# Kernel tuning notes

Hardware: AMD Instinct MI355X
Metric: run time of the kernel (lower is better)

The kernel has to match this reference:

```python
import jax, jax.numpy as jnp
import numpy as np

N, E, HID, HEADS, EDIM = 32768, 262144, 64, 4, 3
C = HID  # per-head out channels (concat=False -> mean over heads)


def setup_inputs() -> dict:
    key = jax.random.key(0)
    ks = jax.random.split(key, 24)
    g = lambda k, shape, s=1.0: jax.random.normal(k, shape, jnp.float32) * s
    s_lin = 1.0 / np.sqrt(HID)
    s_edge = 1.0 / np.sqrt(EDIM)
    s_att = 1.0 / np.sqrt(C)
    inp = {
        "t": jnp.zeros((1,), jnp.float32),
        "h": g(ks[0], (N, HID)),
        "edge_index": jax.random.randint(ks[1], (2, E), 0, N, jnp.int32),
        "edge_attr": g(ks[2], (E, EDIM)),
        "W1": g(ks[3], (HID, HEADS * C), s_lin),
        "We1": g(ks[4], (EDIM, HEADS * C), s_edge),
        "att_src1": g(ks[5], (HEADS, C), s_att),
        "att_dst1": g(ks[6], (HEADS, C), s_att),
        "att_edge1": g(ks[7], (HEADS, C), s_att),
        "b1": jnp.zeros((C,), jnp.float32),
        "ln_g1": jnp.ones((HID,), jnp.float32),
        "ln_b1": jnp.zeros((HID,), jnp.float32),
        # last GAT layer's lin weight is scaled by 0.1 in __init__
        "W2": g(ks[8], (HID, HEADS * C), s_lin) * 0.1,
        "We2": g(ks[9], (EDIM, HEADS * C), s_edge),
        "att_src2": g(ks[10], (HEADS, C), s_att),
        "att_dst2": g(ks[11], (HEADS, C), s_att),
        "att_edge2": g(ks[12], (HEADS, C), s_att),
        "b2": jnp.zeros((C,), jnp.float32),
        "ln_g2": jnp.ones((HID,), jnp.float32),
        "ln_b2": jnp.zeros((HID,), jnp.float32),
    }
    return inp


def _gat_layer(z, src, dst, edge_attr, W, We, a_src, a_dst, a_edge, b):
    # PyG GATConv(edge_dim>0, concat=False, add_self_loops=False), eval mode (no dropout)
    x = (z @ W).reshape(-1, HEADS, C)                      # [N,H,C]
    alpha_s = jnp.einsum("nhc,hc->nh", x, a_src)           # [N,H]
    alpha_d = jnp.einsum("nhc,hc->nh", x, a_dst)           # [N,H]
    e = (edge_attr @ We).reshape(-1, HEADS, C)             # [E,H,C]
    alpha_e = jnp.einsum("ehc,hc->eh", e, a_edge)          # [E,H]
    logit = jax.nn.leaky_relu(alpha_s[src] + alpha_d[dst] + alpha_e, 0.2)  # [E,H]
    # segment softmax over incoming edges of each destination node
    m = jax.lax.stop_gradient(jax.ops.segment_max(logit, dst, num_segments=N))
    ex = jnp.exp(logit - m[dst])
    denom = jax.ops.segment_sum(ex, dst, num_segments=N)
    alpha = ex / (denom[dst] + 1e-16)                      # [E,H]
    msg = x[src] * alpha[..., None]                        # [E,H,C] gather + weight
    out = jax.ops.segment_sum(msg, dst, num_segments=N)    # [N,H,C] scatter-add
    return out.mean(axis=1) + b                            # head mean + bias -> [N,C]


def _layernorm(x, g, b, eps=1e-5):
    mu = x.mean(-1, keepdims=True)
    var = ((x - mu) ** 2).mean(-1, keepdims=True)
    return (x - mu) * jax.lax.rsqrt(var + eps) * g + b


def reference(t, h, edge_index, edge_attr, W1, We1, att_src1, att_dst1, att_edge1, b1,
              ln_g1, ln_b1, W2, We2, att_src2, att_dst2, att_edge2, b2, ln_g2, ln_b2):
    del t  # autonomous ODE func: t unused
    src, dst = edge_index[0], edge_index[1]
    z = h
    z = jax.nn.silu(_layernorm(_gat_layer(z, src, dst, edge_attr, W1, We1, att_src1, att_dst1, att_edge1, b1), ln_g1, ln_b1))
    z = jax.nn.silu(_layernorm(_gat_layer(z, src, dst, edge_attr, W2, We2, att_src2, att_dst2, att_edge2, b2), ln_g2, ln_b2))
    return z
```

## Files before the change

### kernel.cpp

```cpp
#include <hip/hip_runtime.h>
#include <math.h>

#define HIDDEN 64
#define HEADS 4
#define HC 256
#define CAP 64

typedef __attribute__((ext_vector_type(8))) short short8;
typedef __attribute__((ext_vector_type(4))) float f32x4;

__device__ __forceinline__ unsigned short f2bf(float f) {
    unsigned int u = __float_as_uint(f);
    u += 0x7fffu + ((u >> 16) & 1u);
    return (unsigned short)(u >> 16);
}

__device__ __forceinline__ unsigned short f2h(float f) {
    _Float16 h = (_Float16)f;
    return *(unsigned short*)&h;
}

__device__ __forceinline__ float h2f(unsigned int u) {
    unsigned short s = (unsigned short)u;
    _Float16 h = *(_Float16*)&s;
    return (float)h;
}

__device__ __forceinline__ float bflo(unsigned int u) { return __uint_as_float(u << 16); }
__device__ __forceinline__ float bfhi(unsigned int u) { return __uint_as_float(u & 0xffff0000u); }

__global__ __launch_bounds__(256) void k_fused(const int* __restrict__ dst,
                                               const int* __restrict__ src,
                                               const float* __restrict__ ea,
                                               const float* __restrict__ h,
                                               const float* __restrict__ W1f,
                                               const float* __restrict__ W2f,
                                               const float* __restrict__ We1,
                                               const float* __restrict__ ae1,
                                               const float* __restrict__ We2,
                                               const float* __restrict__ ae2,
                                               const float* __restrict__ ats1,
                                               const float* __restrict__ atd1,
                                               const float* __restrict__ ats2,
                                               const float* __restrict__ atd2,
                                               int* __restrict__ counts,
                                               uint2* __restrict__ eb,
                                               ushort* __restrict__ zb,
                                               ushort* __restrict__ wst1,
                                               ushort* __restrict__ wst2,
                                               float* __restrict__ wsv,
                                               float* __restrict__ wr, int E) {
    int t = threadIdx.x, b = blockIdx.x;
    if (b < 1024) {
        int e = b * 256 + t;
        if (e < E) {
            int d = dst[e];
            int c = atomicAdd(&counts[d], 1);
            if (c < CAP) {
                size_t slot = (size_t)d * CAP + c;
                unsigned int lo = (unsigned int)(src[e] & 0xffff)
                                | ((unsigned int)f2h(ea[e * 3 + 0]) << 16);
                unsigned int hi = (unsigned int)f2h(ea[e * 3 + 1])
                                | ((unsigned int)f2h(ea[e * 3 + 2]) << 16);
                eb[slot] = make_uint2(lo, hi);
            }
        }
    } else if (b < 3072) {
        int i = (b - 1024) * 256 + t;
        float4 v = ((const float4*)h)[i];
        ushort4 o;
        o.x = f2bf(v.x); o.y = f2bf(v.y); o.z = f2bf(v.z); o.w = f2bf(v.w);
        ((ushort4*)zb)[i] = o;
    } else if (b < 3200) {
        int j = (b - 3072) * 256 + t;
        const float* W = (j < 16384) ? W1f : W2f;
        ushort* wst = (j < 16384) ? wst1 : wst2;
        int i = j & 16383;
        int c = i >> 8, k = i & 255;
        wst[i] = f2bf(0.25f * W[(k & 63) * HC + (k >> 6) * 64 + c]);
    } else if (b < 3204) {
        int r = b - 3200;
        const float* W = (r >> 1) ? W2f : W1f;
        const float* at;
        if (r == 0) at = ats1; else if (r == 1) at = atd1;
        else if (r == 2) at = ats2; else at = atd2;
        int hh = t >> 6, k = t & 63;
        const float4* wrow = (const float4*)&W[k * HC + hh * 64];
        const float4* arow = (const float4*)&at[hh * 64];
        float v = 0.f;
#pragma unroll
        for (int c4 = 0; c4 < 16; ++c4) {
            float4 wv = wrow[c4], av = arow[c4];
            v += wv.x * av.x + wv.y * av.y + wv.z * av.z + wv.w * av.w;
        }
        wsv[r * 256 + hh * 64 + k] = v;
    } else {
        int wv = t >> 6, lane = t & 63;
#pragma unroll
        for (int it = 0; it < 6; ++it) {
            int comb = wv + it * 4;
            int layer = comb / 12;
            int dh = comb % 12;
            int d = dh >> 2, hh = dh & 3;
            const float* We = layer ? We2 : We1;
            const float* at = layer ? ae2 : ae1;
            float v = We[d * HC + hh * HIDDEN + lane] * at[hh * HIDDEN + lane];
            for (int o = 32; o > 0; o >>= 1) v += __shfl_down(v, o);
            if (lane == 0) wr[layer * 16 + d * HEADS + hh] = v;
        }
    }
}

__global__ __launch_bounds__(256) void k_alpha(const ushort* __restrict__ zb,
                                               const float* __restrict__ wsv,
                                               float* __restrict__ as_,
                                               float* __restrict__ ad_) {
    __shared__ float ls[512];
    int t = threadIdx.x;
    ls[t] = wsv[t];
    ls[t + 256] = wsv[t + 256];
    __syncthreads();
    int n = blockIdx.x * 256 + t;
    const ushort* zr = zb + (size_t)n * HIDDEN;
    float as[4] = {0.f, 0.f, 0.f, 0.f};
    float ad[4] = {0.f, 0.f, 0.f, 0.f};
#pragma unroll
    for (int ks = 0; ks < 8; ++ks) {
        uint4 v = *(const uint4*)(zr + ks * 8);
        unsigned int uu[4] = {v.x, v.y, v.z, v.w};
#pragma unroll
        for (int p = 0; p < 4; ++p) {
            float f0 = bflo(uu[p]), f1 = bfhi(uu[p]);
            int k = ks * 8 + p * 2;
#pragma unroll
            for (int hh = 0; hh < 4; ++hh) {
                as[hh] += f0 * ls[hh * 64 + k] + f1 * ls[hh * 64 + k + 1];
                ad[hh] += f0 * ls[256 + hh * 64 + k] + f1 * ls[256 + hh * 64 + k + 1];
            }
        }
    }
    *(float4*)&as_[n * 4] = make_float4(as[0], as[1], as[2], as[3]);
    *(float4*)&ad_[n * 4] = make_float4(ad[0], ad[1], ad[2], ad[3]);
}

__global__ __launch_bounds__(256) void k_aggregate(
        const ushort* __restrict__ zb, const uint2* __restrict__ eb,
        const int* __restrict__ counts,
        const float* __restrict__ as_, const float* __restrict__ ad_,
        const float* __restrict__ wrl,
        ushort* __restrict__ agg, int N) {
    int lane = threadIdx.x & 63;
    int h = lane >> 4, sub = lane & 15;
    int wid = blockIdx.x * 4 + (threadIdx.x >> 6);
    int nwaves = gridDim.x * 4;
    float w0 = wrl[h], w1 = wrl[4 + h], w2 = wrl[8 + h];

    for (int n = wid; n < N; n += nwaves) {
        int deg = counts[n];
        if (deg > CAP) deg = CAP;
        size_t base = (size_t)n * CAP;
        float ad4 = ad_[n * 4 + h];
        float ssum = 0.f;
        float acc0 = 0.f, acc1 = 0.f, acc2 = 0.f, acc3 = 0.f;

        for (int cs = 0; cs < deg; cs += 16) {
            int idx = cs + sub;
            int s_sub = 0;
            float wgt = 0.f;
            if (idx < deg) {
                uint2 rec = eb[base + idx];
                s_sub = (int)(rec.x & 0xffffu);
                float lg = as_[s_sub * 4 + h] + ad4
                         + h2f(rec.x >> 16) * w0
                         + h2f(rec.y) * w1
                         + h2f(rec.y >> 16) * w2;
                lg = (lg >= 0.f) ? lg : 0.2f * lg;
                wgt = __expf(lg);
            }
            ssum += wgt;

            int jb = deg - cs; if (jb > 16) jb = 16;
            for (int j = 0; j < jb; j += 4) {
                int s_g = __shfl(s_sub, j + h);
                uint2 zv = *(const uint2*)&zb[(size_t)s_g * HIDDEN + sub * 4];
#pragma unroll
                for (int e = 0; e < 4; ++e) {
                    float we = __shfl(wgt, h * 16 + j + e);
                    unsigned int zx = (unsigned int)__shfl((int)zv.x, e * 16 + sub);
                    unsigned int zy = (unsigned int)__shfl((int)zv.y, e * 16 + sub);
                    acc0 += we * bflo(zx);
                    acc1 += we * bfhi(zx);
                    acc2 += we * bflo(zy);
                    acc3 += we * bfhi(zy);
                }
            }
        }
#pragma unroll
        for (int o = 1; o < 16; o <<= 1) ssum += __shfl_xor(ssum, o);
        float winv = 1.f / (ssum + 1e-16f);
        uint2 o2;
        o2.x = (unsigned)f2bf(acc0 * winv) | ((unsigned)f2bf(acc1 * winv) << 16);
        o2.y = (unsigned)f2bf(acc2 * winv) | ((unsigned)f2bf(acc3 * winv) << 16);
        *(uint2*)&agg[(size_t)n * HC + h * 64 + sub * 4] = o2;
    }
}

__global__ __launch_bounds__(256) void k_out(const ushort* __restrict__ agg,
                                             const ushort* __restrict__ wst,
                                             const float* __restrict__ bias,
                                             const float* __restrict__ lng,
                                             const float* __restrict__ lnb,
                                             const float* __restrict__ wsv2,
                                             float* __restrict__ as_,
                                             float* __restrict__ ad_,
                                             float* __restrict__ outf,
                                             ushort* __restrict__ outb) {
    int lane = threadIdx.x & 63;
    int q = lane & 15, quad = lane >> 4;
    int row0 = blockIdx.x * 64 + (threadIdx.x >> 6) * 16;

    const ushort* arow = agg + (size_t)(row0 + q) * HC + quad * 8;
    short8 a[8];
#pragma unroll
    for (int ks = 0; ks < 8; ++ks) a[ks] = *(const short8*)(arow + ks * 32);

    f32x4 acc[4];
#pragma unroll
    for (int nt = 0; nt < 4; ++nt) {
        const ushort* brow = wst + (size_t)(nt * 16 + q) * HC + quad * 8;
        f32x4 c4 = {0.f, 0.f, 0.f, 0.f};
#pragma unroll
        for (int ks = 0; ks < 8; ++ks) {
            short8 bfr = *(const short8*)(brow + ks * 32);
            c4 = __builtin_amdgcn_mfma_f32_16x16x32_bf16(a[ks], bfr, c4, 0, 0, 0);
        }
        acc[nt] = c4;
    }

    float u[4][4], s1[4] = {0.f, 0.f, 0.f, 0.f};
#pragma unroll
    for (int nt = 0; nt < 4; ++nt) {
        float bv = bias[nt * 16 + q];
#pragma unroll
        for (int r = 0; r < 4; ++r) { u[nt][r] = acc[nt][r] + bv; s1[r] += u[nt][r]; }
    }
#pragma unroll
    for (int o = 1; o < 16; o <<= 1)
#pragma unroll
        for (int r = 0; r < 4; ++r) s1[r] += __shfl_xor(s1[r], o);
    float mu[4], s2[4] = {0.f, 0.f, 0.f, 0.f};
#pragma unroll
    for (int r = 0; r < 4; ++r) mu[r] = s1[r] * (1.f / 64.f);
#pragma unroll
    for (int nt = 0; nt < 4; ++nt)
#pragma unroll
        for (int r = 0; r < 4; ++r) { float d = u[nt][r] - mu[r]; s2[r] += d * d; }
#pragma unroll
    for (int o = 1; o < 16; o <<= 1)
#pragma unroll
        for (int r = 0; r < 4; ++r) s2[r] += __shfl_xor(s2[r], o);
    float rstd[4];
#pragma unroll
    for (int r = 0; r < 4; ++r) rstd[r] = rsqrtf(s2[r] * (1.f / 64.f) + 1e-5f);

    float rv[4][4];
#pragma unroll
    for (int nt = 0; nt < 4; ++nt) {
        float gv = lng[nt * 16 + q], bb = lnb[nt * 16 + q];
#pragma unroll
        for (int r = 0; r < 4; ++r) {
            float y = (u[nt][r] - mu[r]) * rstd[r] * gv + bb;
            rv[nt][r] = y / (1.f + __expf(-y));
        }
    }

    if (outb) {
#pragma unroll
        for (int nt = 0; nt < 4; ++nt)
#pragma unroll
            for (int r = 0; r < 4; ++r)
                outb[(size_t)(row0 + quad * 4 + r) * HIDDEN + nt * 16 + q] = f2bf(rv[nt][r]);
        float vs[4][4] = {{0.f}}, vd[4][4] = {{0.f}};
#pragma unroll
        for (int hh = 0; hh < 4; ++hh)
#pragma unroll
            for (int nt = 0; nt < 4; ++nt) {
                float wsc = wsv2[hh * 64 + nt * 16 + q];
                float wdc = wsv2[256 + hh * 64 + nt * 16 + q];
#pragma unroll
                for (int r = 0; r < 4; ++r) {
                    vs[r][hh] += rv[nt][r] * wsc;
                    vd[r][hh] += rv[nt][r] * wdc;
                }
            }
#pragma unroll
        for (int o = 1; o < 16; o <<= 1)
#pragma unroll
            for (int r = 0; r < 4; ++r)
#pragma unroll
                for (int hh = 0; hh < 4; ++hh) {
                    vs[r][hh] += __shfl_xor(vs[r][hh], o);
                    vd[r][hh] += __shfl_xor(vd[r][hh], o);
                }
        if (q < 4) {
#pragma unroll
            for (int r = 0; r < 4; ++r) {
                float sv = (q == 0) ? vs[r][0] : (q == 1) ? vs[r][1]
                         : (q == 2) ? vs[r][2] : vs[r][3];
                float dv = (q == 0) ? vd[r][0] : (q == 1) ? vd[r][1]
                         : (q == 2) ? vd[r][2] : vd[r][3];
                int n = row0 + quad * 4 + r;
                as_[n * 4 + q] = sv;
                ad_[n * 4 + q] = dv;
            }
        }
    } else {
#pragma unroll
        for (int nt = 0; nt < 4; ++nt)
#pragma unroll
            for (int r = 0; r < 4; ++r)
                outf[(size_t)(row0 + quad * 4 + r) * HIDDEN + nt * 16 + q] = rv[nt][r];
    }
}


extern "C" void kernel_launch(void* const* d_in, const int* in_sizes, int n_in,
                              void* d_out, int out_size, void* d_ws, size_t ws_size,
                              hipStream_t stream) {
    const float* h   = (const float*)d_in[1];
    const int*   ei  = (const int*)d_in[2];
    const float* ea  = (const float*)d_in[3];
    const float* W1  = (const float*)d_in[4];
    const float* We1 = (const float*)d_in[5];
    const float* as1 = (const float*)d_in[6];
    const float* ad1 = (const float*)d_in[7];
    const float* ae1 = (const float*)d_in[8];
    const float* b1  = (const float*)d_in[9];
    const float* lg1 = (const float*)d_in[10];
    const float* lb1 = (const float*)d_in[11];
    const float* W2  = (const float*)d_in[12];
    const float* We2 = (const float*)d_in[13];
    const float* as2 = (const float*)d_in[14];
    const float* ad2 = (const float*)d_in[15];
    const float* ae2 = (const float*)d_in[16];
    const float* b2  = (const float*)d_in[17];
    const float* lg2 = (const float*)d_in[18];
    const float* lb2 = (const float*)d_in[19];

    const int N = in_sizes[1] / HIDDEN;
    const int E = in_sizes[2] / 2;
    const int* srcp = ei;
    const int* dstp = ei + E;

    char* w = (char*)d_ws;
    ushort* agg   = (ushort*)w; w += (size_t)N * HC * 2;
    ushort* zb    = (ushort*)w; w += (size_t)N * HIDDEN * 2;
    float* as_    = (float*)w;  w += (size_t)N * HEADS * 4;
    float* adv    = (float*)w;  w += (size_t)N * HEADS * 4;
    ushort* wst1  = (ushort*)w; w += 16384 * 2;
    ushort* wst2  = (ushort*)w; w += 16384 * 2;
    float* wsv    = (float*)w;  w += 1024 * 4;
    float* wr     = (float*)w;  w += 128;
    int* counts   = (int*)w;    w += (size_t)N * 4;
    uint2* eb     = (uint2*)w;  w += (size_t)N * CAP * 8;

    hipMemsetAsync(counts, 0, (size_t)N * 4, stream);
    k_fused<<<3205, 256, 0, stream>>>(dstp, srcp, ea, h, W1, W2,
                                      We1, ae1, We2, ae2,
                                      as1, ad1, as2, ad2,
                                      counts, eb, zb, wst1, wst2, wsv, wr, E);

    k_alpha<<<N / 256, 256, 0, stream>>>(zb, wsv, as_, adv);
    k_aggregate<<<4096, 256, 0, stream>>>(zb, eb, counts, as_, adv, wr, agg, N);
    k_out<<<N / 64, 256, 0, stream>>>(agg, wst1, b1, lg1, lb1, wsv + 512,
                                      as_, adv, nullptr, zb);
    k_aggregate<<<4096, 256, 0, stream>>>(zb, eb, counts, as_, adv, wr + 16, agg, N);
    k_out<<<N / 64, 256, 0, stream>>>(agg, wst2, b2, lg2, lb2, nullptr,
                                      nullptr, nullptr, (float*)d_out, nullptr);
}
```

Baseline: 194.0 us.

## Fuse edge aggregation with output projection and LayerNorm via shared-memory tile

Merges the aggregate and output kernels into one kernel per layer. Each block aggregates 16 nodes into an LDS tile, then one wave runs the MFMA projection, LayerNorm, SiLU and next-layer alpha computation. This drops the large global agg buffer write and read, and ping-pongs the z and alpha buffers so the fused kernel can run without read/write hazards. The aggregation inner loop also changes: each lane now gathers one neighbor row per step and accumulates all four heads, followed by cross-head shuffle reductions. Only one of four waves does the epilogue, so MFMA work is serialized per block and occupancy may be limited by the launch bound.

```diff
diff --git a/kernel.cpp b/kernel.cpp
--- a/kernel.cpp
+++ b/kernel.cpp
@@ -143,25 +143,46 @@
     *(float4*)&ad_[n * 4] = make_float4(ad[0], ad[1], ad[2], ad[3]);
 }
 
-__global__ __launch_bounds__(256) void k_aggregate(
+__global__ __launch_bounds__(256, 4) void k_aggout(
         const ushort* __restrict__ zb, const uint2* __restrict__ eb,
         const int* __restrict__ counts,
         const float* __restrict__ as_, const float* __restrict__ ad_,
         const float* __restrict__ wrl,
-        ushort* __restrict__ agg, int N) {
+        const ushort* __restrict__ wst, const float* __restrict__ bias,
+        const float* __restrict__ lng, const float* __restrict__ lnb,
+        const float* __restrict__ wsv2,
+        float* __restrict__ as2, float* __restrict__ ad2,
+        float* __restrict__ outf, ushort* __restrict__ outb, int N) {
+    __shared__ ushort sagg[16][264];
     int lane = threadIdx.x & 63;
+    int wave = threadIdx.x >> 6;
     int h = lane >> 4, sub = lane & 15;
-    int wid = blockIdx.x * 4 + (threadIdx.x >> 6);
-    int nwaves = gridDim.x * 4;
+    int nbase = blockIdx.x * 16;
+
     float w0 = wrl[h], w1 = wrl[4 + h], w2 = wrl[8 + h];
 
-    for (int n = wid; n < N; n += nwaves) {
-        int deg = counts[n];
-        if (deg > CAP) deg = CAP;
+    int degs[4]; float ad4s[4];
+#pragma unroll
+    for (int i = 0; i < 4; ++i) {
+        int n = nbase + wave * 4 + i;
+        int d = counts[n];
+        degs[i] = (d > CAP) ? CAP : d;
+        ad4s[i] = ad_[(size_t)n * 4 + h];
+    }
+
+#pragma unroll
+    for (int i = 0; i < 4; ++i) {
+        int nl = wave * 4 + i;
+        int n = nbase + nl;
+        int deg = degs[i];
         size_t base = (size_t)n * CAP;
-        float ad4 = ad_[n * 4 + h];
+        float ad4 = ad4s[i];
         float ssum = 0.f;
-        float acc0 = 0.f, acc1 = 0.f, acc2 = 0.f, acc3 = 0.f;
+        float acc[4][4];
+#pragma unroll
+        for (int a = 0; a < 4; ++a)
+#pragma unroll
+            for (int j = 0; j < 4; ++j) acc[a][j] = 0.f;
 
         for (int cs = 0; cs < deg; cs += 16) {
             int idx = cs + sub;
@@ -170,7 +191,7 @@
             if (idx < deg) {
                 uint2 rec = eb[base + idx];
                 s_sub = (int)(rec.x & 0xffffu);
-                float lg = as_[s_sub * 4 + h] + ad4
+                float lg = as_[(size_t)s_sub * 4 + h] + ad4
                          + h2f(rec.x >> 16) * w0
                          + h2f(rec.y) * w1
                          + h2f(rec.y >> 16) * w2;
@@ -180,146 +201,148 @@
             ssum += wgt;
 
             int jb = deg - cs; if (jb > 16) jb = 16;
-            for (int j = 0; j < jb; j += 4) {
-                int s_g = __shfl(s_sub, j + h);
+            for (int j4 = 0; j4 < jb; j4 += 4) {
+                int eidx = j4 + h;
+                int s_g = __shfl(s_sub, eidx);
                 uint2 zv = *(const uint2*)&zb[(size_t)s_g * HIDDEN + sub * 4];
-#pragma unroll
-                for (int e = 0; e < 4; ++e) {
-                    float we = __shfl(wgt, h * 16 + j + e);
-                    unsigned int zx = (unsigned int)__shfl((int)zv.x, e * 16 + sub);
-                    unsigned int zy = (unsigned int)__shfl((int)zv.y, e * 16 + sub);
-                    acc0 += we * bflo(zx);
-                    acc1 += we * bfhi(zx);
-                    acc2 += we * bflo(zy);
-                    acc3 += we * bfhi(zy);
+                float z0 = bflo(zv.x), z1 = bfhi(zv.x);
+                float z2v = bflo(zv.y), z3 = bfhi(zv.y);
+#pragma unroll
+                for (int hh = 0; hh < 4; ++hh) {
+                    float wh = __shfl(wgt, hh * 16 + eidx);
+                    acc[hh][0] += wh * z0;
+                    acc[hh][1] += wh * z1;
+                    acc[hh][2] += wh * z2v;
+                    acc[hh][3] += wh * z3;
                 }
             }
         }
 #pragma unroll
         for (int o = 1; o < 16; o <<= 1) ssum += __shfl_xor(ssum, o);
         float winv = 1.f / (ssum + 1e-16f);
-        uint2 o2;
-        o2.x = (unsigned)f2bf(acc0 * winv) | ((unsigned)f2bf(acc1 * winv) << 16);
-        o2.y = (unsigned)f2bf(acc2 * winv) | ((unsigned)f2bf(acc3 * winv) << 16);
-        *(uint2*)&agg[(size_t)n * HC + h * 64 + sub * 4] = o2;
+#pragma unroll
+        for (int a = 0; a < 4; ++a)
+#pragma unroll
+            for (int j = 0; j < 4; ++j) {
+                acc[a][j] += __shfl_xor(acc[a][j], 16);
+                acc[a][j] += __shfl_xor(acc[a][j], 32);
+            }
+        float sel[4];
+#pragma unroll
+        for (int j = 0; j < 4; ++j)
+            sel[j] = (h == 0) ? acc[0][j] : (h == 1) ? acc[1][j]
+                   : (h == 2) ? acc[2][j] : acc[3][j];
+        uint2 pk;
+        pk.x = (unsigned)f2bf(sel[0] * winv) | ((unsigned)f2bf(sel[1] * winv) << 16);
+        pk.y = (unsigned)f2bf(sel[2] * winv) | ((unsigned)f2bf(sel[3] * winv) << 16);
+        *(uint2*)&sagg[nl][h * 64 + sub * 4] = pk;
     }
-}
-
-__global__ __launch_bounds__(256) void k_out(const ushort* __restrict__ agg,
-                                             const ushort* __restrict__ wst,
-                                             const float* __restrict__ bias,
-                                             const float* __restrict__ lng,
-                                             const float* __restrict__ lnb,
-                                             const float* __restrict__ wsv2,
-                                             float* __restrict__ as_,
-                                             float* __restrict__ ad_,
-                                             float* __restrict__ outf,
-                                             ushort* __restrict__ outb) {
-    int lane = threadIdx.x & 63;
-    int q = lane & 15, quad = lane >> 4;
-    int row0 = blockIdx.x * 64 + (threadIdx.x >> 6) * 16;
-
-    const ushort* arow = agg + (size_t)(row0 + q) * HC + quad * 8;
-    short8 a[8];
-#pragma unroll
-    for (int ks = 0; ks < 8; ++ks) a[ks] = *(const short8*)(arow + ks * 32);
-
-    f32x4 acc[4];
-#pragma unroll
-    for (int nt = 0; nt < 4; ++nt) {
-        const ushort* brow = wst + (size_t)(nt * 16 + q) * HC + quad * 8;
-        f32x4 c4 = {0.f, 0.f, 0.f, 0.f};
-#pragma unroll
-        for (int ks = 0; ks < 8; ++ks) {
-            short8 bfr = *(const short8*)(brow + ks * 32);
-            c4 = __builtin_amdgcn_mfma_f32_16x16x32_bf16(a[ks], bfr, c4, 0, 0, 0);
-        }
-        acc[nt] = c4;
-    }
-
-    float u[4][4], s1[4] = {0.f, 0.f, 0.f, 0.f};
-#pragma unroll
-    for (int nt = 0; nt < 4; ++nt) {
-        float bv = bias[nt * 16 + q];
-#pragma unroll
-        for (int r = 0; r < 4; ++r) { u[nt][r] = acc[nt][r] + bv; s1[r] += u[nt][r]; }
-    }
-#pragma unroll
-    for (int o = 1; o < 16; o <<= 1)
-#pragma unroll
-        for (int r = 0; r < 4; ++r) s1[r] += __shfl_xor(s1[r], o);
-    float mu[4], s2[4] = {0.f, 0.f, 0.f, 0.f};
-#pragma unroll
-    for (int r = 0; r < 4; ++r) mu[r] = s1[r] * (1.f / 64.f);
-#pragma unroll
-    for (int nt = 0; nt < 4; ++nt)
-#pragma unroll
-        for (int r = 0; r < 4; ++r) { float d = u[nt][r] - mu[r]; s2[r] += d * d; }
-#pragma unroll
-    for (int o = 1; o < 16; o <<= 1)
-#pragma unroll
-        for (int r = 0; r < 4; ++r) s2[r] += __shfl_xor(s2[r], o);
-    float rstd[4];
-#pragma unroll
-    for (int r = 0; r < 4; ++r) rstd[r] = rsqrtf(s2[r] * (1.f / 64.f) + 1e-5f);
-
-    float rv[4][4];
-#pragma unroll
-    for (int nt = 0; nt < 4; ++nt) {
-        float gv = lng[nt * 16 + q], bb = lnb[nt * 16 + q];
-#pragma unroll
-        for (int r = 0; r < 4; ++r) {
-            float y = (u[nt][r] - mu[r]) * rstd[r] * gv + bb;
-            rv[nt][r] = y / (1.f + __expf(-y));
-        }
-    }
-
-    if (outb) {
+    __syncthreads();
+
+    if (wave == 0) {
+        int q = lane & 15, quad = lane >> 4;
+        short8 a[8];
+#pragma unroll
+        for (int ks = 0; ks < 8; ++ks)
+            a[ks] = *(const short8*)&sagg[q][quad * 8 + ks * 32];
+
+        f32x4 acc[4];
+#pragma unroll
+        for (int nt = 0; nt < 4; ++nt) {
+            const ushort* brow = wst + (size_t)(nt * 16 + q) * HC + quad * 8;
+            f32x4 c4 = {0.f, 0.f, 0.f, 0.f};
+#pragma unroll
+            for (int ks = 0; ks < 8; ++ks) {
+                short8 bfr = *(const short8*)(brow + ks * 32);
+                c4 = __builtin_amdgcn_mfma_f32_16x16x32_bf16(a[ks], bfr, c4, 0, 0, 0);
+            }
+            acc[nt] = c4;
+        }
+
+        float u[4][4], s1[4] = {0.f, 0.f, 0.f, 0.f};
+#pragma unroll
+        for (int nt = 0; nt < 4; ++nt) {
+            float bv = bias[nt * 16 + q];
+#pragma unroll
+            for (int r = 0; r < 4; ++r) { u[nt][r] = acc[nt][r] + bv; s1[r] += u[nt][r]; }
+        }
+#pragma unroll
+        for (int o = 1; o < 16; o <<= 1)
+#pragma unroll
+            for (int r = 0; r < 4; ++r) s1[r] += __shfl_xor(s1[r], o);
+        float mu[4], s2[4] = {0.f, 0.f, 0.f, 0.f};
+#pragma unroll
+        for (int r = 0; r < 4; ++r) mu[r] = s1[r] * (1.f / 64.f);
 #pragma unroll
         for (int nt = 0; nt < 4; ++nt)
 #pragma unroll
-            for (int r = 0; r < 4; ++r)
-                outb[(size_t)(row0 + quad * 4 + r) * HIDDEN + nt * 16 + q] = f2bf(rv[nt][r]);
-        float vs[4][4] = {{0.f}}, vd[4][4] = {{0.f}};
-#pragma unroll
-        for (int hh = 0; hh < 4; ++hh)
-#pragma unroll
-            for (int nt = 0; nt < 4; ++nt) {
-                float wsc = wsv2[hh * 64 + nt * 16 + q];
-                float wdc = wsv2[256 + hh * 64 + nt * 16 + q];
+            for (int r = 0; r < 4; ++r) { float d = u[nt][r] - mu[r]; s2[r] += d * d; }
+#pragma unroll
+        for (int o = 1; o < 16; o <<= 1)
+#pragma unroll
+            for (int r = 0; r < 4; ++r) s2[r] += __shfl_xor(s2[r], o);
+        float rstd[4];
+#pragma unroll
+        for (int r = 0; r < 4; ++r) rstd[r] = rsqrtf(s2[r] * (1.f / 64.f) + 1e-5f);
+
+        float rv[4][4];
+#pragma unroll
+        for (int nt = 0; nt < 4; ++nt) {
+            float gv = lng[nt * 16 + q], bb = lnb[nt * 16 + q];
+#pragma unroll
+            for (int r = 0; r < 4; ++r) {
+                float y = (u[nt][r] - mu[r]) * rstd[r] * gv + bb;
+                rv[nt][r] = y / (1.f + __expf(-y));
+            }
+        }
+
+        if (outb) {
+#pragma unroll
+            for (int nt = 0; nt < 4; ++nt)
+#pragma unroll
+                for (int r = 0; r < 4; ++r)
+                    outb[(size_t)(nbase + quad * 4 + r) * HIDDEN + nt * 16 + q] = f2bf(rv[nt][r]);
+            float vs[4][4] = {{0.f}}, vd[4][4] = {{0.f}};
+#pragma unroll
+            for (int hh = 0; hh < 4; ++hh)
+#pragma unroll
+                for (int nt = 0; nt < 4; ++nt) {
+                    float wsc = wsv2[hh * 64 + nt * 16 + q];
+                    float wdc = wsv2[256 + hh * 64 + nt * 16 + q];
+#pragma unroll
+                    for (int r = 0; r < 4; ++r) {
+                        vs[r][hh] += rv[nt][r] * wsc;
+                        vd[r][hh] += rv[nt][r] * wdc;
+                    }
+                }
+#pragma unroll
+            for (int o = 1; o < 16; o <<= 1)
+#pragma unroll
+                for (int r = 0; r < 4; ++r)
+#pragma unroll
+                    for (int hh = 0; hh < 4; ++hh) {
+                        vs[r][hh] += __shfl_xor(vs[r][hh], o);
+                        vd[r][hh] += __shfl_xor(vd[r][hh], o);
+                    }
+            if (q < 4) {
 #pragma unroll
                 for (int r = 0; r < 4; ++r) {
-                    vs[r][hh] += rv[nt][r] * wsc;
-                    vd[r][hh] += rv[nt][r] * wdc;
+                    float sv = (q == 0) ? vs[r][0] : (q == 1) ? vs[r][1]
+                             : (q == 2) ? vs[r][2] : vs[r][3];
+                    float dv = (q == 0) ? vd[r][0] : (q == 1) ? vd[r][1]
+                             : (q == 2) ? vd[r][2] : vd[r][3];
+                    int n = nbase + quad * 4 + r;
+                    as2[(size_t)n * 4 + q] = sv;
+                    ad2[(size_t)n * 4 + q] = dv;
                 }
             }
-#pragma unroll
-        for (int o = 1; o < 16; o <<= 1)
-#pragma unroll
-            for (int r = 0; r < 4; ++r)
-#pragma unroll
-                for (int hh = 0; hh < 4; ++hh) {
-                    vs[r][hh] += __shfl_xor(vs[r][hh], o);
-                    vd[r][hh] += __shfl_xor(vd[r][hh], o);
-                }
-        if (q < 4) {
-#pragma unroll
-            for (int r = 0; r < 4; ++r) {
-                float sv = (q == 0) ? vs[r][0] : (q == 1) ? vs[r][1]
-                         : (q == 2) ? vs[r][2] : vs[r][3];
-                float dv = (q == 0) ? vd[r][0] : (q == 1) ? vd[r][1]
-                         : (q == 2) ? vd[r][2] : vd[r][3];
-                int n = row0 + quad * 4 + r;
-                as_[n * 4 + q] = sv;
-                ad_[n * 4 + q] = dv;
-            }
-        }
-    } else {
-#pragma unroll
-        for (int nt = 0; nt < 4; ++nt)
-#pragma unroll
-            for (int r = 0; r < 4; ++r)
-                outf[(size_t)(row0 + quad * 4 + r) * HIDDEN + nt * 16 + q] = rv[nt][r];
+        } else {
+#pragma unroll
+            for (int nt = 0; nt < 4; ++nt)
+#pragma unroll
+                for (int r = 0; r < 4; ++r)
+                    outf[(size_t)(nbase + quad * 4 + r) * HIDDEN + nt * 16 + q] = rv[nt][r];
+        }
     }
 }
 
@@ -353,10 +376,12 @@
     const int* dstp = ei + E;
 
     char* w = (char*)d_ws;
-    ushort* agg   = (ushort*)w; w += (size_t)N * HC * 2;
     ushort* zb    = (ushort*)w; w += (size_t)N * HIDDEN * 2;
+    ushort* zb2   = (ushort*)w; w += (size_t)N * HIDDEN * 2;
     float* as_    = (float*)w;  w += (size_t)N * HEADS * 4;
     float* adv    = (float*)w;  w += (size_t)N * HEADS * 4;
+    float* as2_   = (float*)w;  w += (size_t)N * HEADS * 4;
+    float* ad2_   = (float*)w;  w += (size_t)N * HEADS * 4;
     ushort* wst1  = (ushort*)w; w += 16384 * 2;
     ushort* wst2  = (ushort*)w; w += 16384 * 2;
     float* wsv    = (float*)w;  w += 1024 * 4;
@@ -371,10 +396,11 @@
                                       counts, eb, zb, wst1, wst2, wsv, wr, E);
 
     k_alpha<<<N / 256, 256, 0, stream>>>(zb, wsv, as_, adv);
-    k_aggregate<<<4096, 256, 0, stream>>>(zb, eb, counts, as_, adv, wr, agg, N);
-    k_out<<<N / 64, 256, 0, stream>>>(agg, wst1, b1, lg1, lb1, wsv + 512,
-                                      as_, adv, nullptr, zb);
-    k_aggregate<<<4096, 256, 0, stream>>>(zb, eb, counts, as_, adv, wr + 16, agg, N);
-    k_out<<<N / 64, 256, 0, stream>>>(agg, wst2, b2, lg2, lb2, nullptr,
-                                      nullptr, nullptr, (float*)d_out, nullptr);
-}
+
+    k_aggout<<<N / 16, 256, 0, stream>>>(zb, eb, counts, as_, adv, wr,
+                                         wst1, b1, lg1, lb1, wsv + 512,
+                                         as2_, ad2_, nullptr, zb2, N);
+    k_aggout<<<N / 16, 256, 0, stream>>>(zb2, eb, counts, as2_, ad2_, wr + 16,
+                                         wst2, b2, lg2, lb2, nullptr,
+                                         nullptr, nullptr, (float*)d_out, nullptr, N);
+}
```

After: 189.5 us. 1.02x faster.
